# Kernel optimization log

Measured on AMD Instinct MI355X. Metric: run time of the kernel, lower is better.

The kernel has to match this reference:

```python
import jax, jax.numpy as jnp
import numpy as np

TEMPERATURE = 0.05
REDUCTION = "mean"
EPS = 1e-12

B, LQ, LK, D = 128, 256, 512, 1024


def l2_normalize(x):
    # torch F.normalize: x / clamp(||x||_2, min=eps)
    n = jnp.sqrt(jnp.sum(x * x, axis=-1, keepdims=True))
    return x / jnp.maximum(n, EPS)


def setup_inputs() -> dict:
    key = jax.random.key(0)
    k1, k2, k3, k4, k5, k6 = jax.random.split(key, 6)
    return {
        "query": jax.random.normal(k1, (B, LQ, D), dtype=jnp.float32),
        "pos_key": jax.random.normal(k2, (B, LK, D), dtype=jnp.float32),
        "neg_key": jax.random.normal(k3, (B, LK, D), dtype=jnp.float32),
        "query_mask": jax.random.randint(k4, (B, LQ), 0, 2, dtype=jnp.int32),
        "pos_mask": jax.random.randint(k5, (B, LK), 0, 2, dtype=jnp.int32),
        "neg_mask": jax.random.randint(k6, (B, LK), 0, 2, dtype=jnp.int32),
    }


def _maxsim_logit(q, k, k_mask, q_mask):
    # q: [B, Lq, D] (normalized), k: [B, Lk, D] (normalized)
    sim = jnp.einsum("bqd,bkd->bqk", q, k)  # [B, Lq, Lk]
    sim = sim * k_mask[:, None, :].astype(sim.dtype)  # mask keys (multiplicative, as in source)
    m = jnp.max(sim, axis=-1)  # [B, Lq]
    return jnp.sum(m * q_mask.astype(m.dtype), axis=-1, keepdims=True)  # [B, 1]


def reference(query, pos_key, neg_key, query_mask, pos_mask, neg_mask):
    q = l2_normalize(query)
    pk = l2_normalize(pos_key)
    nk = l2_normalize(neg_key)
    pos_logit = _maxsim_logit(q, pk, pos_mask, query_mask)  # [B, 1]
    neg_logit = _maxsim_logit(q, nk, neg_mask, query_mask)  # [B, 1]
    logits = jnp.concatenate([pos_logit, neg_logit], axis=1) / TEMPERATURE  # [B, 2]
    # cross-entropy with target class 0
    logp = jax.nn.log_softmax(logits, axis=-1)
    nll = -logp[:, 0]  # [B]
    if REDUCTION == "mean":
        return jnp.mean(nll)
    elif REDUCTION == "sum":
        return jnp.sum(nll)
    return nll
```

## Files before the change

kernel.cpp:

```cpp
#include <hip/hip_runtime.h>
#include <hip/hip_fp16.h>
#include <math.h>


constexpr int NB = 128;
constexpr int LQ = 256;
constexpr int LK = 512;
constexpr int DD = 1024;

#define TEMP_INV 20.0f
#define EPSN 1e-12f

typedef __fp16 fp16x2 __attribute__((ext_vector_type(2)));
typedef _Float16 f16x8 __attribute__((ext_vector_type(8)));
typedef float f32x4 __attribute__((ext_vector_type(4)));

#define BM 128
#define BN 128
#define BK 64
#define KITERS (DD / BK)

__device__ inline f16x8 cvt8(float4 a, float4 b) {
  union { f16x8 v; fp16x2 h[4]; } u;
  u.h[0] = __builtin_amdgcn_cvt_pkrtz(a.x, a.y);
  u.h[1] = __builtin_amdgcn_cvt_pkrtz(a.z, a.w);
  u.h[2] = __builtin_amdgcn_cvt_pkrtz(b.x, b.y);
  u.h[3] = __builtin_amdgcn_cvt_pkrtz(b.z, b.w);
  return u.v;
}

__global__ __launch_bounds__(512, 4) void maxsim_kernel(
    const float* __restrict__ q, const float* __restrict__ pk,
    const float* __restrict__ nk, const int* __restrict__ pmask,
    const int* __restrict__ nmask, float* __restrict__ part) {
  __shared__ _Float16 __align__(16) As[2][BM * BK];
  __shared__ _Float16 __align__(16) Bs[2][BN * BK];

  const int bid = blockIdx.x;
  const int sw = (bid & 7) * 256 + (bid >> 3);
  const int b = sw >> 4;
  const int x = sw & 15;
  const int mt = x >> 3;
  const int nt = (x >> 1) & 3;
  const int kt = x & 1;

  const float* kbase = kt ? nk : pk;
  const int* mbase = kt ? nmask : pmask;

  const float* Ag = q + ((size_t)b * LQ + mt * BM) * DD;
  const float* Bg = kbase + ((size_t)b * LK + nt * BN) * DD;

  const int tid = threadIdx.x;
  const int lane = tid & 63;
  const int w = tid >> 6;
  const int wr = w >> 1;
  const int wc = w & 1;
  const int frow = lane & 15;
  const int kgrp = lane >> 4;

  const int srow0 = tid >> 3;
  const int sc = tid & 7;

  const float* pa[2];
  const float* pb[2];
  #pragma unroll
  for (int i = 0; i < 2; ++i) {
    pa[i] = Ag + (size_t)(srow0 + 64 * i) * DD + sc * 8;
    pb[i] = Bg + (size_t)(srow0 + 64 * i) * DD + sc * 8;
  }

  float ssqA[2] = {0.f, 0.f};
  float ssqB[2] = {0.f, 0.f};
  f32x4 acc[2][4] = {};

  auto LOADS = [&](int it, float4 (&ra)[2][2], float4 (&rb)[2][2]) {
    const int koff = it * BK;
    #pragma unroll
    for (int i = 0; i < 2; ++i) {
      ra[i][0] = *(const float4*)(pa[i] + koff);
      ra[i][1] = *(const float4*)(pa[i] + koff + 4);
      rb[i][0] = *(const float4*)(pb[i] + koff);
      rb[i][1] = *(const float4*)(pb[i] + koff + 4);
    }
  };
  auto STORE = [&](int bsel, float4 (&ra)[2][2], float4 (&rb)[2][2]) {
    #pragma unroll
    for (int i = 0; i < 2; ++i) {
      float4 a0 = ra[i][0], a1 = ra[i][1], b0 = rb[i][0], b1 = rb[i][1];
      ssqA[i] += a0.x * a0.x + a0.y * a0.y + a0.z * a0.z + a0.w * a0.w +
                 a1.x * a1.x + a1.y * a1.y + a1.z * a1.z + a1.w * a1.w;
      ssqB[i] += b0.x * b0.x + b0.y * b0.y + b0.z * b0.z + b0.w * b0.w +
                 b1.x * b1.x + b1.y * b1.y + b1.z * b1.z + b1.w * b1.w;
      const int row = srow0 + 64 * i;
      const int cofs = ((sc ^ (row & 7)) << 3);
      *(f16x8*)&As[bsel][row * BK + cofs] = cvt8(a0, a1);
      *(f16x8*)&Bs[bsel][row * BK + cofs] = cvt8(b0, b1);
    }
  };
  auto COMPUTE = [&](int bsel) {
    __builtin_amdgcn_s_setprio(1);
    #pragma unroll
    for (int ks = 0; ks < 2; ++ks) {
      const int ch = ks * 4 + kgrp;
      f16x8 af[2], bf[4];
      #pragma unroll
      for (int m = 0; m < 2; ++m) {
        const int row = wr * 32 + m * 16 + frow;
        af[m] = *(const f16x8*)&As[bsel][row * BK + ((ch ^ (row & 7)) << 3)];
      }
      #pragma unroll
      for (int n = 0; n < 4; ++n) {
        const int row = wc * 64 + n * 16 + frow;
        bf[n] = *(const f16x8*)&Bs[bsel][row * BK + ((ch ^ (row & 7)) << 3)];
      }
      #pragma unroll
      for (int m = 0; m < 2; ++m)
        #pragma unroll
        for (int n = 0; n < 4; ++n)
          acc[m][n] = __builtin_amdgcn_mfma_f32_16x16x32_f16(af[m], bf[n], acc[m][n], 0, 0, 0);
    }
    __builtin_amdgcn_s_setprio(0);
  };

  {
    float4 ca[2][2], cb[2][2];
    LOADS(0, ca, cb);
    STORE(0, ca, cb);
  }
  __syncthreads();

  #pragma unroll
  for (int it = 0; it < KITERS - 1; ++it) {
    float4 na[2][2], nb[2][2];
    LOADS(it + 1, na, nb);
    __builtin_amdgcn_sched_barrier(0);
    COMPUTE(it & 1);
    STORE((it & 1) ^ 1, na, nb);
    __syncthreads();
  }
  COMPUTE(1);

  #pragma unroll
  for (int off = 1; off < 8; off <<= 1) {
    #pragma unroll
    for (int i = 0; i < 2; ++i) {
      ssqA[i] += __shfl_xor(ssqA[i], off);
      ssqB[i] += __shfl_xor(ssqB[i], off);
    }
  }

  float* const aux = reinterpret_cast<float*>(&As[0][0]);
  float* const cs = aux;
  float* const invA_s = aux + BN;
  float* const rmax = aux + BN + BM;

  if (sc == 0) {
    #pragma unroll
    for (int i = 0; i < 2; ++i) {
      const int row = srow0 + 64 * i;
      invA_s[row] = 1.0f / fmaxf(sqrtf(ssqA[i]), EPSN);
      const int key = nt * BN + row;
      const float mk = mbase[(size_t)b * LK + key] ? 1.0f : 0.0f;
      cs[row] = mk / fmaxf(sqrtf(ssqB[i]), EPSN);
    }
  }
  __syncthreads();

  float vmax[2][4];
  #pragma unroll
  for (int m = 0; m < 2; ++m)
    #pragma unroll
    for (int r = 0; r < 4; ++r) vmax[m][r] = -INFINITY;
  #pragma unroll
  for (int n = 0; n < 4; ++n) {
    const float s = cs[wc * 64 + n * 16 + frow];
    #pragma unroll
    for (int m = 0; m < 2; ++m)
      #pragma unroll
      for (int r = 0; r < 4; ++r)
        vmax[m][r] = fmaxf(vmax[m][r], acc[m][n][r] * s);
  }
  #pragma unroll
  for (int off = 1; off < 16; off <<= 1)
    #pragma unroll
    for (int m = 0; m < 2; ++m)
      #pragma unroll
      for (int r = 0; r < 4; ++r)
        vmax[m][r] = fmaxf(vmax[m][r], __shfl_xor(vmax[m][r], off));
  if ((lane & 15) == 0) {
    #pragma unroll
    for (int m = 0; m < 2; ++m)
      #pragma unroll
      for (int r = 0; r < 4; ++r)
        rmax[(wr * 32 + m * 16 + kgrp * 4 + r) * 2 + wc] = vmax[m][r];
  }
  __syncthreads();
  if (tid < BM) {
    const float v = fmaxf(rmax[tid * 2], rmax[tid * 2 + 1]) * invA_s[tid];
    part[(((size_t)kt * NB + b) * 4 + nt) * LQ + mt * BM + tid] = v;
  }
}

__global__ __launch_bounds__(256) void logits_kernel(
    const float* __restrict__ part, const int* __restrict__ qmask,
    float* __restrict__ nll) {
  int b = blockIdx.x;
  int t = threadIdx.x;
  float mp = -INFINITY, mn = -INFINITY;
  #pragma unroll
  for (int ntile = 0; ntile < 4; ++ntile) {
    mp = fmaxf(mp, part[(((size_t)0 * NB + b) * 4 + ntile) * LQ + t]);
    mn = fmaxf(mn, part[(((size_t)1 * NB + b) * 4 + ntile) * LQ + t]);
  }
  float qm = qmask[(size_t)b * LQ + t] ? 1.0f : 0.0f;
  float p = mp * qm;
  float n = mn * qm;
  #pragma unroll
  for (int o = 32; o; o >>= 1) { p += __shfl_down(p, o); n += __shfl_down(n, o); }
  __shared__ float sp[4], sn[4];
  int lane = t & 63, w = t >> 6;
  if (lane == 0) { sp[w] = p; sn[w] = n; }
  __syncthreads();
  if (t == 0) {
    float ps = sp[0] + sp[1] + sp[2] + sp[3];
    float ns = sn[0] + sn[1] + sn[2] + sn[3];
    float z = (ns - ps) * TEMP_INV;
    nll[b] = z > 0.0f ? z + log1pf(expf(-z)) : log1pf(expf(z));
  }
}

__global__ void finalize_kernel(const float* __restrict__ nll, float* __restrict__ out) {
  __shared__ float s[128];
  int t = threadIdx.x;
  s[t] = nll[t];
  __syncthreads();
  #pragma unroll
  for (int o = 64; o; o >>= 1) {
    if (t < o) s[t] += s[t + o];
    __syncthreads();
  }
  if (t == 0) out[0] = s[0] * (1.0f / 128.0f);
}

extern "C" void kernel_launch(void* const* d_in, const int* in_sizes, int n_in,
                              void* d_out, int out_size, void* d_ws, size_t ws_size,
                              hipStream_t stream) {
  const float* q = (const float*)d_in[0];
  const float* pk = (const float*)d_in[1];
  const float* nk = (const float*)d_in[2];
  const int* qm = (const int*)d_in[3];
  const int* pm = (const int*)d_in[4];
  const int* nm = (const int*)d_in[5];

  float* ws = (float*)d_ws;
  float* part = ws;
  float* nll = part + 262144;

  maxsim_kernel<<<2048, 512, 0, stream>>>(q, pk, nk, pm, nm, part);
  logits_kernel<<<NB, 256, 0, stream>>>(part, qm, nll);
  finalize_kernel<<<1, 128, 0, stream>>>(nll, (float*)d_out);
}
```

Before: 183.8 us.

## Halve K-tile to 32 with paired-row swizzled LDS layout

Reduces the K tile from 64 to 32, so each thread loads one row chunk per stage instead of two. LDS tiles use a new paired-row XOR swizzle to avoid bank conflicts. The smaller stage lowers register and LDS pressure and may raise occupancy. In exchange it doubles the number of K iterations and barriers, and each barrier interval has less MFMA work to hide global latency.

```diff
diff --git a/kernel.cpp b/kernel.cpp
--- a/kernel.cpp
+++ b/kernel.cpp
@@ -17,7 +17,7 @@
 
 #define BM 128
 #define BN 128
-#define BK 64
+#define BK 32
 #define KITERS (DD / BK)
 
 __device__ inline f16x8 cvt8(float4 a, float4 b) {
@@ -29,6 +29,12 @@
   return u.v;
 }
 
+__device__ __forceinline__ int lidx(int row, int ch) {
+  const int line = row >> 1;
+  const int slot = ((ch | ((row & 1) << 2)) ^ (line & 7));
+  return line * 64 + slot * 8;
+}
+
 __global__ __launch_bounds__(512, 4) void maxsim_kernel(
     const float* __restrict__ q, const float* __restrict__ pk,
     const float* __restrict__ nk, const int* __restrict__ pmask,
@@ -58,111 +64,78 @@
   const int frow = lane & 15;
   const int kgrp = lane >> 4;
 
-  const int srow0 = tid >> 3;
-  const int sc = tid & 7;
-
-  const float* pa[2];
-  const float* pb[2];
-  #pragma unroll
-  for (int i = 0; i < 2; ++i) {
-    pa[i] = Ag + (size_t)(srow0 + 64 * i) * DD + sc * 8;
-    pb[i] = Bg + (size_t)(srow0 + 64 * i) * DD + sc * 8;
-  }
-
-  float ssqA[2] = {0.f, 0.f};
-  float ssqB[2] = {0.f, 0.f};
+  const int rowS = tid >> 2;
+  const int chS = tid & 3;
+  const float* pA = Ag + (size_t)rowS * DD + chS * 8;
+  const float* pB = Bg + (size_t)rowS * DD + chS * 8;
+  const int sidx = lidx(rowS, chS);
+
+  float ssqA = 0.f, ssqB = 0.f;
   f32x4 acc[2][4] = {};
 
-  auto LOADS = [&](int it, float4 (&ra)[2][2], float4 (&rb)[2][2]) {
+  auto LOADS = [&](int it, float4& a0, float4& a1, float4& b0, float4& b1) {
     const int koff = it * BK;
-    #pragma unroll
-    for (int i = 0; i < 2; ++i) {
-      ra[i][0] = *(const float4*)(pa[i] + koff);
-      ra[i][1] = *(const float4*)(pa[i] + koff + 4);
-      rb[i][0] = *(const float4*)(pb[i] + koff);
-      rb[i][1] = *(const float4*)(pb[i] + koff + 4);
-    }
+    a0 = *(const float4*)(pA + koff);
+    a1 = *(const float4*)(pA + koff + 4);
+    b0 = *(const float4*)(pB + koff);
+    b1 = *(const float4*)(pB + koff + 4);
   };
-  auto STORE = [&](int bsel, float4 (&ra)[2][2], float4 (&rb)[2][2]) {
-    #pragma unroll
-    for (int i = 0; i < 2; ++i) {
-      float4 a0 = ra[i][0], a1 = ra[i][1], b0 = rb[i][0], b1 = rb[i][1];
-      ssqA[i] += a0.x * a0.x + a0.y * a0.y + a0.z * a0.z + a0.w * a0.w +
-                 a1.x * a1.x + a1.y * a1.y + a1.z * a1.z + a1.w * a1.w;
-      ssqB[i] += b0.x * b0.x + b0.y * b0.y + b0.z * b0.z + b0.w * b0.w +
-                 b1.x * b1.x + b1.y * b1.y + b1.z * b1.z + b1.w * b1.w;
-      const int row = srow0 + 64 * i;
-      const int cofs = ((sc ^ (row & 7)) << 3);
-      *(f16x8*)&As[bsel][row * BK + cofs] = cvt8(a0, a1);
-      *(f16x8*)&Bs[bsel][row * BK + cofs] = cvt8(b0, b1);
-    }
+  auto STORE = [&](int bsel, float4 a0, float4 a1, float4 b0, float4 b1) {
+    ssqA += a0.x * a0.x + a0.y * a0.y + a0.z * a0.z + a0.w * a0.w +
+            a1.x * a1.x + a1.y * a1.y + a1.z * a1.z + a1.w * a1.w;
+    ssqB += b0.x * b0.x + b0.y * b0.y + b0.z * b0.z + b0.w * b0.w +
+            b1.x * b1.x + b1.y * b1.y + b1.z * b1.z + b1.w * b1.w;
+    *(f16x8*)&As[bsel][sidx] = cvt8(a0, a1);
+    *(f16x8*)&Bs[bsel][sidx] = cvt8(b0, b1);
   };
   auto COMPUTE = [&](int bsel) {
     __builtin_amdgcn_s_setprio(1);
-    #pragma unroll
-    for (int ks = 0; ks < 2; ++ks) {
-      const int ch = ks * 4 + kgrp;
-      f16x8 af[2], bf[4];
-      #pragma unroll
-      for (int m = 0; m < 2; ++m) {
-        const int row = wr * 32 + m * 16 + frow;
-        af[m] = *(const f16x8*)&As[bsel][row * BK + ((ch ^ (row & 7)) << 3)];
-      }
-      #pragma unroll
-      for (int n = 0; n < 4; ++n) {
-        const int row = wc * 64 + n * 16 + frow;
-        bf[n] = *(const f16x8*)&Bs[bsel][row * BK + ((ch ^ (row & 7)) << 3)];
-      }
-      #pragma unroll
-      for (int m = 0; m < 2; ++m)
-        #pragma unroll
-        for (int n = 0; n < 4; ++n)
-          acc[m][n] = __builtin_amdgcn_mfma_f32_16x16x32_f16(af[m], bf[n], acc[m][n], 0, 0, 0);
-    }
+    f16x8 af[2], bf[4];
+    #pragma unroll
+    for (int m = 0; m < 2; ++m)
+      af[m] = *(const f16x8*)&As[bsel][lidx(wr * 32 + m * 16 + frow, kgrp)];
+    #pragma unroll
+    for (int n = 0; n < 4; ++n)
+      bf[n] = *(const f16x8*)&Bs[bsel][lidx(wc * 64 + n * 16 + frow, kgrp)];
+    #pragma unroll
+    for (int m = 0; m < 2; ++m)
+      #pragma unroll
+      for (int n = 0; n < 4; ++n)
+        acc[m][n] = __builtin_amdgcn_mfma_f32_16x16x32_f16(af[m], bf[n], acc[m][n], 0, 0, 0);
     __builtin_amdgcn_s_setprio(0);
   };
 
   {
-    float4 ca[2][2], cb[2][2];
-    LOADS(0, ca, cb);
-    STORE(0, ca, cb);
+    float4 a0, a1, b0, b1;
+    LOADS(0, a0, a1, b0, b1);
+    STORE(0, a0, a1, b0, b1);
   }
   __syncthreads();
 
   #pragma unroll
   for (int it = 0; it < KITERS - 1; ++it) {
-    float4 na[2][2], nb[2][2];
-    LOADS(it + 1, na, nb);
+    float4 a0, a1, b0, b1;
+    LOADS(it + 1, a0, a1, b0, b1);
     __builtin_amdgcn_sched_barrier(0);
     COMPUTE(it & 1);
-    STORE((it & 1) ^ 1, na, nb);
+    STORE((it & 1) ^ 1, a0, a1, b0, b1);
     __syncthreads();
   }
   COMPUTE(1);
 
-  #pragma unroll
-  for (int off = 1; off < 8; off <<= 1) {
-    #pragma unroll
-    for (int i = 0; i < 2; ++i) {
-      ssqA[i] += __shfl_xor(ssqA[i], off);
-      ssqB[i] += __shfl_xor(ssqB[i], off);
-    }
-  }
+  ssqA += __shfl_xor(ssqA, 1); ssqA += __shfl_xor(ssqA, 2);
+  ssqB += __shfl_xor(ssqB, 1); ssqB += __shfl_xor(ssqB, 2);
 
   float* const aux = reinterpret_cast<float*>(&As[0][0]);
-  float* const cs = aux;
+  float* const csc = aux;
   float* const invA_s = aux + BN;
   float* const rmax = aux + BN + BM;
 
-  if (sc == 0) {
-    #pragma unroll
-    for (int i = 0; i < 2; ++i) {
-      const int row = srow0 + 64 * i;
-      invA_s[row] = 1.0f / fmaxf(sqrtf(ssqA[i]), EPSN);
-      const int key = nt * BN + row;
-      const float mk = mbase[(size_t)b * LK + key] ? 1.0f : 0.0f;
-      cs[row] = mk / fmaxf(sqrtf(ssqB[i]), EPSN);
-    }
+  if (chS == 0) {
+    invA_s[rowS] = 1.0f / fmaxf(sqrtf(ssqA), EPSN);
+    const int key = nt * BN + rowS;
+    csc[rowS] = (mbase[(size_t)b * LK + key] ? 1.0f : 0.0f) /
+                fmaxf(sqrtf(ssqB), EPSN);
   }
   __syncthreads();
 
@@ -173,7 +146,7 @@
     for (int r = 0; r < 4; ++r) vmax[m][r] = -INFINITY;
   #pragma unroll
   for (int n = 0; n < 4; ++n) {
-    const float s = cs[wc * 64 + n * 16 + frow];
+    const float s = csc[wc * 64 + n * 16 + frow];
     #pragma unroll
     for (int m = 0; m < 2; ++m)
       #pragma unroll
```

Measured after the change: 180.9 us (median of 2 runs). No clear change (-1.6%).
